# Performance work log

Measured on AMD Instinct MI355X. Metric: run time of the kernel, lower is better.

Reference implementation:

```python
import jax, jax.numpy as jnp
import numpy as np

D, IN_CH, H, W = 4, 13, 384, 384
EMBED, HID, N_COLORS = 64, 32, 11


def conv(x, w, b, stride=1, pad=0):
    y = jax.lax.conv_general_dilated(
        x, w, window_strides=(stride, stride),
        padding=[(pad, pad), (pad, pad)],
        dimension_numbers=('NCHW', 'OIHW', 'NCHW'))
    return y + b[None, :, None, None]


def setup_inputs() -> dict:
    key = jax.random.key(0)
    ks = jax.random.split(key, 16)
    s = 0.05
    return {
        'demo_inputs': jax.random.normal(ks[0], (D, IN_CH, H, W), jnp.float32),
        'demo_outputs': jax.random.normal(ks[1], (D, IN_CH, H, W), jnp.float32),
        'test_input': jax.random.normal(ks[2], (IN_CH, H, W), jnp.float32),
        'enc_w1': jax.random.normal(ks[3], (32, 26, 3, 3), jnp.float32) * s,
        'enc_b1': jnp.zeros((32,), jnp.float32),
        'enc_w2': jax.random.normal(ks[4], (64, 32, 3, 3), jnp.float32) * s,
        'enc_b2': jnp.zeros((64,), jnp.float32),
        'enc_w3': jax.random.normal(ks[5], (64, 64, 3, 3), jnp.float32) * s,
        'enc_b3': jnp.zeros((64,), jnp.float32),
        'enc_lw': jax.random.normal(ks[6], (EMBED, 64), jnp.float32) * s,
        'enc_lb': jnp.zeros((EMBED,), jnp.float32),
        'stem_w': jax.random.normal(ks[7], (HID, IN_CH, 3, 3), jnp.float32) * s,
        'stem_b': jnp.zeros((HID,), jnp.float32),
        'upd_w1': jax.random.normal(ks[8], (HID, HID + EMBED, 3, 3), jnp.float32) * s,
        'upd_b1': jnp.zeros((HID,), jnp.float32),
        'upd_w2': jax.random.normal(ks[9], (HID, HID, 1, 1), jnp.float32) * s,
        'upd_b2': jnp.zeros((HID,), jnp.float32),
        'tau_w': jax.random.normal(ks[10], (HID, HID + EMBED, 1, 1), jnp.float32) * s,
        'tau_b': jnp.zeros((HID,), jnp.float32),
        'dec_w': jax.random.normal(ks[11], (N_COLORS, HID, 1, 1), jnp.float32) * s,
        'dec_b': jnp.zeros((N_COLORS,), jnp.float32),
        'n_steps': 8,
    }


def reference(demo_inputs, demo_outputs, test_input,
              enc_w1, enc_b1, enc_w2, enc_b2, enc_w3, enc_b3, enc_lw, enc_lb,
              stem_w, stem_b, upd_w1, upd_b1, upd_w2, upd_b2,
              tau_w, tau_b, dec_w, dec_b, n_steps):
    # encode_demos: concat each (in, out) pair along channels -> [D, 2*in_ch, H, W]
    pairs = jnp.concatenate([demo_inputs, demo_outputs], axis=1)
    h = jax.nn.relu(conv(pairs, enc_w1, enc_b1, stride=1, pad=1))
    h = jax.nn.relu(conv(h, enc_w2, enc_b2, stride=2, pad=1))
    h = jax.nn.relu(conv(h, enc_w3, enc_b3, stride=2, pad=1))
    h = h.mean(axis=(2, 3))                      # AdaptiveAvgPool2d(1) + Flatten -> [D, 64]
    emb = h @ enc_lw.T + enc_lb                  # [D, embed_dim]
    task_embed = emb.mean(axis=0)                # [embed_dim]

    x = test_input[None]                         # [1, in_ch, H, W]
    Hh, Ww = x.shape[2], x.shape[3]
    te = jnp.broadcast_to(task_embed[None, :, None, None], (1, task_embed.shape[0], Hh, Ww))
    state = jax.nn.relu(conv(x, stem_w, stem_b, stride=1, pad=1))
    for _ in range(n_steps):
        ctx = jnp.concatenate([state, te], axis=1)   # [1, hid+embed, H, W]
        delta = conv(jax.nn.relu(conv(ctx, upd_w1, upd_b1, stride=1, pad=1)),
                     upd_w2, upd_b2, stride=1, pad=0)
        beta = jax.nn.sigmoid(conv(ctx, tau_w, tau_b, stride=1, pad=0))
        state = beta * state + (1.0 - beta) * delta
    return conv(state, dec_w, dec_b, stride=1, pad=0)  # [1, N_COLORS, H, W]
```

## Files before the change

### kernel.cpp

```cpp
#include <hip/hip_runtime.h>

#define HW 147456

typedef __attribute__((ext_vector_type(8))) short bf16x8;
typedef __attribute__((ext_vector_type(4))) float f32x4;

__device__ __forceinline__ float bf2f(unsigned short u) {
    return __uint_as_float(((unsigned)u) << 16);
}
__device__ __forceinline__ unsigned short f2bf(float f) {
    unsigned u = __float_as_uint(f);
    return (unsigned short)((u + 0x7fffu + ((u >> 16) & 1u)) >> 16);
}

struct TJobs {
    const float* src[5];
    float* dst[5];
    int cout[5], cintot[5], k[5], coutp[5];
    int start[6];
};

__global__ __launch_bounds__(256) void transpose_all_k(TJobs J) {
    int gid = blockIdx.x * 256 + threadIdx.x;
    if (gid >= J.start[5]) return;
    int j = 0;
#pragma unroll
    for (int t = 1; t < 5; ++t)
        if (gid >= J.start[t]) j = t;
    int li = gid - J.start[j];
    int coutp = J.coutp[j], K = J.k[j];
    int co = li % coutp;
    int kk = (li / coutp) % K;
    int cin = li / (coutp * K);
    J.dst[j][li] = (co < J.cout[j]) ? J.src[j][((co * J.cintot[j]) + cin) * K + kk] : 0.f;
}

struct WJobs {
    const float* src[4];
    unsigned short* dst[4];
    int cout[4], cin[4], cintot[4], cinp[4];
    int start[5];
};

__global__ __launch_bounds__(256) void transpose_wbf_k(WJobs J) {
    int gid = blockIdx.x * 256 + threadIdx.x;
    if (gid >= J.start[4]) return;
    int j = 0;
#pragma unroll
    for (int t = 1; t < 4; ++t)
        if (gid >= J.start[t]) j = t;
    int li = gid - J.start[j];
    int cinp = J.cinp[j];
    int ci = li % cinp;
    int co = (li / cinp) % J.cout[j];
    int tap = li / (cinp * J.cout[j]);
    float v = (ci < J.cin[j]) ? J.src[j][((co * J.cintot[j]) + ci) * 9 + tap] : 0.f;
    J.dst[j][li] = f2bf(v);
}

template <int CIN, int CP, int COUT, int S, int OX, int OY, int MW, bool RELU>
__global__ __launch_bounds__(256, MW) void mfma_conv_k(
    const float* __restrict__ in0, const float* __restrict__ in1, int split,
    long off0base, long off1base, long zs0, long zs1, int inW, int inH,
    const unsigned short* __restrict__ wB,
    const float* __restrict__ bias,
    float* __restrict__ out, long outZS) {
    constexpr int XT = (OX - 1) * S + 3;
    constexpr int YT = (OY - 1) * S + 3;
    constexpr int CINK = (CIN + 31) & ~31;
    constexpr int KST = CINK / 32;
    constexpr int NCG = COUT / 16;
    constexpr int NTX = OX / 16;
    constexpr int NSP = NTX * OY;
    constexpr int NTASK = NSP * NCG;
    constexpr int NT4 = NTASK / 4;
    constexpr int NSLOT = YT * XT;
    static_assert(NTASK % 4 == 0, "tasks per wave");
    static_assert(NSP % NT4 == 0, "wave must own a single cout-group");
    static_assert(CP % 8 == 0 && CP >= CINK, "LDS cin pad");
    static_assert((CP / 8) % 2 == 1, "odd chunk stride for bank spread");
    __shared__ __align__(16) unsigned short tile[NSLOT * CP];
    const int tid = threadIdx.x;
    const int bx = blockIdx.x, by = blockIdx.y, z = blockIdx.z;
    const long o0 = off0base + (long)z * zs0;
    const long o1 = off1base + (long)z * zs1;
    const int outW = inW / S, outH = inH / S;
    const int gx0 = bx * OX * S - 1;
    const int gy0 = by * OY * S - 1;

#pragma unroll 1
    for (int s = tid; s < NSLOT; s += 256) {
        const int sy = s / XT;
        const int lx = s - sy * XT;
        const int gy = gy0 + sy;
        const int gx = gx0 + lx;
        const bool ok = ((unsigned)gy < (unsigned)inH) && ((unsigned)gx < (unsigned)inW);
        const long pix = (long)gy * inW + gx;
#pragma unroll
        for (int h = 0; h < CINK / 8; ++h) {
            bf16x8 v;
#pragma unroll
            for (int e = 0; e < 8; ++e) {
                const int c = h * 8 + e;
                float f = 0.f;
                if (c < CIN && ok) {
                    const float* base = (c < split)
                        ? in0 + o0 + (long)c * inH * inW
                        : in1 + o1 + (long)(c - split) * inH * inW;
                    f = base[pix];
                }
                v[e] = (short)f2bf(f);
            }
            *(bf16x8*)(tile + s * CP + h * 8) = v;
        }
    }
    __syncthreads();

    const int wv = tid >> 6;
    const int l = tid & 63;
    const int ln = l & 15;
    const int lk = l >> 4;
    const int cg = (wv * NT4) / NSP;
    bf16x8 bfr[9 * KST];
#pragma unroll
    for (int tap = 0; tap < 9; ++tap)
#pragma unroll
        for (int h = 0; h < KST; ++h)
            bfr[tap * KST + h] = *(const bf16x8*)(wB + ((long)(tap * COUT + cg * 16 + ln)) * CINK + h * 32 + lk * 8);
    const float bv = bias[cg * 16 + ln];
#pragma unroll 1
    for (int t = 0; t < NT4; ++t) {
        const int sp = wv * NT4 + t - cg * NSP;
        const int tx = sp % NTX;
        const int ty = sp / NTX;
        f32x4 acc;
        acc[0] = bv; acc[1] = bv; acc[2] = bv; acc[3] = bv;
#pragma unroll
        for (int ky = 0; ky < 3; ++ky) {
#pragma unroll
            for (int kx = 0; kx < 3; ++kx) {
                const int yb = ty * S + ky;
                const int xb = (tx * 16 + ln) * S + kx;
                const unsigned short* ap = tile + (yb * XT + xb) * CP + lk * 8;
#pragma unroll
                for (int h = 0; h < KST; ++h) {
                    bf16x8 a = *(const bf16x8*)(ap + h * 32);
                    acc = __builtin_amdgcn_mfma_f32_16x16x32_bf16(a, bfr[(ky * 3 + kx) * KST + h], acc, 0, 0, 0);
                }
            }
        }
        const int ox = bx * OX + tx * 16 + lk * 4;
        const int oy = by * OY + ty;
        float4 o;
        if constexpr (RELU) {
            o.x = fmaxf(acc[0], 0.f);
            o.y = fmaxf(acc[1], 0.f);
            o.z = fmaxf(acc[2], 0.f);
            o.w = fmaxf(acc[3], 0.f);
        } else {
            o.x = acc[0]; o.y = acc[1]; o.z = acc[2]; o.w = acc[3];
        }
        *(float4*)(out + (long)z * outZS + ((long)(cg * 16 + ln) * outH + oy) * outW + ox) = o;
    }
}

template <int CIN, int CCHUNK, int WCH, int COUT, int STRIDE, int TW, int CO_PER, int MW>
__global__ __launch_bounds__(256, MW) void conv3x3_k(
    const float* __restrict__ in0, const float* __restrict__ in1, int split,
    long inOff0, long inOff1, long zs0, long zs1, int inW, int inH,
    const float* __restrict__ wT, const float* __restrict__ bias,
    float* __restrict__ out, long outZS) {
    constexpr int NCG = COUT / CO_PER;
    constexpr int NPXG = 256 / NCG;
    constexpr int NXG = TW / 4;
    constexpr int TH = NPXG / NXG;
    constexpr int INW = (TW - 1) * STRIDE + 3;
    constexpr int INH = (TH - 1) * STRIDE + 3;
    constexpr int WIN = 3 * STRIDE + 3;
    constexpr int XV = (INW + 6) / 4;
    constexpr int LDSW = XV * 4 + 1;
    constexpr int SLOTS = INH * XV;
    static_assert(NPXG % NXG == 0 && NPXG * NCG == 256, "thread mapping");
    static_assert(CIN % CCHUNK == 0 && CCHUNK % WCH == 0, "chunking");
    static_assert(SLOTS <= 256, "staging slots");
    __shared__ float tile[CCHUNK][INH][LDSW];
    __shared__ __align__(16) float wlds[WCH * 9 * COUT];
    const int tid = threadIdx.x;
    const int cg = tid / NPXG;
    const int pg = tid % NPXG;
    const int xg = pg % NXG;
    const int yy = pg / NXG;
    const int bx = blockIdx.x, by = blockIdx.y, z = blockIdx.z;
    const int outW = inW / STRIDE, outH = inH / STRIDE;
    const long off0 = inOff0 + (long)z * zs0;
    const long off1 = inOff1 + (long)z * zs1;
    float* outp = out + (long)z * outZS;
    const bool sact = tid < SLOTS;
    const int sr = tid / XV;
    const int sx = tid - sr * XV;
    const int gxs = bx * TW * STRIDE - 4 + sx * 4;
    const int gy0 = by * TH * STRIDE - 1;

    float acc[4][CO_PER];
    {
        float bv[CO_PER];
#pragma unroll
        for (int jj = 0; jj < CO_PER; jj += 4) {
            float4 b4 = *(const float4*)(bias + cg * CO_PER + jj);
            bv[jj] = b4.x; bv[jj + 1] = b4.y; bv[jj + 2] = b4.z; bv[jj + 3] = b4.w;
        }
#pragma unroll
        for (int p = 0; p < 4; ++p)
#pragma unroll
            for (int j = 0; j < CO_PER; ++j) acc[p][j] = bv[j];
    }

    for (int ch = 0; ch < CIN; ch += CCHUNK) {
        if (sact) {
            const int gy = gy0 + sr;
            const bool yok = (unsigned)gy < (unsigned)inH;
            const bool xfull = (gxs >= 0) && (gxs + 3 < inW);
#pragma unroll
            for (int c = 0; c < CCHUNK; ++c) {
                const int gc = ch + c;
                const float* row = (gc < split)
                    ? in0 + off0 + ((long)gc * inH + gy) * inW
                    : in1 + off1 + ((long)(gc - split) * inH + gy) * inW;
                float4 v = {0.f, 0.f, 0.f, 0.f};
                if (yok) {
                    if (xfull) {
                        v = *(const float4*)(row + gxs);
                    } else {
                        float t[4];
#pragma unroll
                        for (int k = 0; k < 4; ++k) {
                            int gx = gxs + k;
                            t[k] = ((unsigned)gx < (unsigned)inW) ? row[gx] : 0.f;
                        }
                        v = {t[0], t[1], t[2], t[3]};
                    }
                }
                float* dst = &tile[c][sr][sx * 4];
                dst[0] = v.x; dst[1] = v.y; dst[2] = v.z; dst[3] = v.w;
            }
        }
#pragma unroll 1
        for (int wc = 0; wc < CCHUNK; wc += WCH) {
            {
                const float4* wsrc = (const float4*)(wT + (long)(ch + wc) * 9 * COUT);
                float4* wdst = (float4*)wlds;
                constexpr int CNT = WCH * 9 * COUT / 4;
                for (int i = tid; i < CNT; i += 256) wdst[i] = wsrc[i];
            }
            __syncthreads();
#pragma unroll 1
            for (int c = 0; c < WCH; ++c) {
#pragma unroll
                for (int ky = 0; ky < 3; ++ky) {
                    const int ty = yy * STRIDE + ky;
                    const int tx0 = xg * 4 * STRIDE + 3;
                    float xw[WIN];
#pragma unroll
                    for (int i = 0; i < WIN; ++i) xw[i] = tile[wc + c][ty][tx0 + i];
#pragma unroll
                    for (int dx = 0; dx < 3; ++dx) {
                        const float* wp = wlds + ((c * 3 + ky) * 3 + dx) * COUT + cg * CO_PER;
                        float wv[CO_PER];
#pragma unroll
                        for (int jj = 0; jj < CO_PER; jj += 4) {
                            float4 w4 = *(const float4*)(wp + jj);
                            wv[jj] = w4.x; wv[jj + 1] = w4.y; wv[jj + 2] = w4.z; wv[jj + 3] = w4.w;
                        }
#pragma unroll
                        for (int p = 0; p < 4; ++p) {
                            float xv = xw[p * STRIDE + dx];
#pragma unroll
                            for (int j = 0; j < CO_PER; ++j) acc[p][j] = fmaf(xv, wv[j], acc[p][j]);
                        }
                    }
                }
            }
            __syncthreads();
        }
    }

    const int ox0 = bx * TW + xg * 4;
    const int oy = by * TH + yy;
#pragma unroll
    for (int j = 0; j < CO_PER; ++j) {
        int co = cg * CO_PER + j;
        float4 o;
        o.x = fmaxf(acc[0][j], 0.f);
        o.y = fmaxf(acc[1][j], 0.f);
        o.z = fmaxf(acc[2][j], 0.f);
        o.w = fmaxf(acc[3][j], 0.f);
        *(float4*)(outp + ((long)co * outH + oy) * outW + ox0) = o;
    }
}

__global__ __launch_bounds__(256) void pool_k(const float* __restrict__ enc3base,
                                              long zstride,
                                              float* __restrict__ meanout) {
    int z = blockIdx.x >> 6;
    int c = blockIdx.x & 63;
    const float* p = enc3base + (long)z * zstride + (long)c * 9216;
    float s = 0.f;
    for (int i = threadIdx.x; i < 9216; i += 256) s += p[i];
    __shared__ float red[256];
    red[threadIdx.x] = s;
    __syncthreads();
    for (int o = 128; o > 0; o >>= 1) {
        if (threadIdx.x < o) red[threadIdx.x] += red[threadIdx.x + o];
        __syncthreads();
    }
    if (threadIdx.x == 0) meanout[z * 64 + c] = red[0] * (1.f / 9216.f);
}

__global__ __launch_bounds__(256) void prep_te_k(
    const float* __restrict__ means, const float* __restrict__ lw,
    const float* __restrict__ lb, const float* __restrict__ tauw,
    const float* __restrict__ taub, const float* __restrict__ w1,
    const float* __restrict__ b1,
    float* __restrict__ tauc, float* __restrict__ wsum,
    float* __restrict__ bias2) {
    __shared__ float tes[64];
    int t = threadIdx.x;
    if (t < 64) {
        float s = 0.f;
        for (int d = 0; d < 4; ++d)
            for (int c = 0; c < 64; ++c) s += means[d * 64 + c] * lw[t * 64 + c];
        tes[t] = lb[t] + 0.25f * s;
    }
    __syncthreads();
    if (t < 32) {
        float s = taub[t];
        for (int e = 0; e < 64; ++e) s += tauw[t * 96 + 32 + e] * tes[e];
        tauc[t] = s;
    }
    for (int i = t; i < 288; i += 256) {
        int co = i % 32;
        int k = i / 32;
        float s = 0.f;
        for (int e = 0; e < 64; ++e) s += w1[((co * 96) + 32 + e) * 9 + k] * tes[e];
        wsum[i] = s;
    }
    __syncthreads();
    if (t < 32) {
        float s = b1[t];
        for (int k = 0; k < 9; ++k) s += wsum[k * 32 + t];
        bias2[t] = s;
    }
}

__global__ __launch_bounds__(256, 4) void nca_fuse_k(
    const float* __restrict__ sold, float* __restrict__ hb,
    const float* __restrict__ wsum, const float* __restrict__ w2T,
    const float* __restrict__ b2, const float* __restrict__ tauT,
    const float* __restrict__ tauc) {
    __shared__ unsigned short h1s[32][136];
    __shared__ __align__(16) float ss[32][132];
    __shared__ __align__(16) float sw2[1024];
    __shared__ __align__(16) float stu[1024];
    __shared__ float swv[288], sb2[32], stc[32];
    const int tid = threadIdx.x;
    const long px0 = (long)blockIdx.x * 128;
    for (int i = tid; i < 1024; i += 256) {
        sw2[i] = w2T[i];
        stu[i] = tauT[i];
    }
    for (int i = tid; i < 288; i += 256) swv[i] = wsum[i];
    if (tid < 32) {
        sb2[tid] = b2[tid];
        stc[tid] = tauc[tid];
    }
    const int yrow = (int)(px0 / 384);
    const int xbase = (int)(px0 - (long)yrow * 384);
    const bool ytop = (yrow == 0), ybot = (yrow == 383);
#pragma unroll 1
    for (int i = tid; i < 1024; i += 256) {
        const int ch = i >> 5;
        const int p4 = i & 31;
        float4 h4 = *(const float4*)(hb + (long)ch * HW + px0 + p4 * 4);
        float4 s4 = *(const float4*)(sold + (long)ch * HW + px0 + p4 * 4);
        float hv[4] = {h4.x, h4.y, h4.z, h4.w};
        unsigned short ho[4];
#pragma unroll
        for (int e = 0; e < 4; ++e) {
            const int x = xbase + p4 * 4 + e;
            float h = hv[e];
            const bool xl = (x == 0), xr = (x == 383);
            if (xl | xr | ytop | ybot) {
#pragma unroll
                for (int ky = 0; ky < 3; ++ky)
#pragma unroll
                    for (int kx = 0; kx < 3; ++kx) {
                        bool inval = (ky == 0 && ytop) || (ky == 2 && ybot) ||
                                     (kx == 0 && xl) || (kx == 2 && xr);
                        if (inval) h -= swv[(ky * 3 + kx) * 32 + ch];
                    }
            }
            ho[e] = f2bf(fmaxf(h, 0.f));
        }
        unsigned short* hd = &h1s[ch][p4 * 4];
        hd[0] = ho[0]; hd[1] = ho[1]; hd[2] = ho[2]; hd[3] = ho[3];
        *(float4*)(&ss[ch][p4 * 4]) = s4;
    }
    __syncthreads();

    const int cg = tid >> 5;
    const int pg = tid & 31;
    const int p0 = pg * 4;
    float accd[4][4], acct[4][4];
    {
        float dv[4], tv[4];
#pragma unroll
        for (int j = 0; j < 4; ++j) {
            dv[j] = sb2[cg * 4 + j];
            tv[j] = stc[cg * 4 + j];
        }
#pragma unroll
        for (int p = 0; p < 4; ++p)
#pragma unroll
            for (int j = 0; j < 4; ++j) { accd[p][j] = dv[j]; acct[p][j] = tv[j]; }
    }
#pragma unroll 2
    for (int ci = 0; ci < 32; ++ci) {
        float hv[4], sv[4];
#pragma unroll
        for (int p = 0; p < 4; ++p) {
            hv[p] = bf2f(h1s[ci][p0 + p]);
            sv[p] = ss[ci][p0 + p];
        }
        float4 wd4 = *(const float4*)(sw2 + ci * 32 + cg * 4);
        float4 wt4 = *(const float4*)(stu + ci * 32 + cg * 4);
        float wdv[4] = {wd4.x, wd4.y, wd4.z, wd4.w};
        float wtv[4] = {wt4.x, wt4.y, wt4.z, wt4.w};
#pragma unroll
        for (int p = 0; p < 4; ++p) {
#pragma unroll
            for (int j = 0; j < 4; ++j) {
                accd[p][j] = fmaf(hv[p], wdv[j], accd[p][j]);
                acct[p][j] = fmaf(sv[p], wtv[j], acct[p][j]);
            }
        }
    }
#pragma unroll
    for (int j = 0; j < 4; ++j) {
        const int co = cg * 4 + j;
        float ov[4];
#pragma unroll
        for (int p = 0; p < 4; ++p) {
            float sown = ss[co][p0 + p];
            float beta = 1.f / (1.f + __expf(-acct[p][j]));
            ov[p] = beta * sown + (1.f - beta) * accd[p][j];
        }
        float4 o = {ov[0], ov[1], ov[2], ov[3]};
        *(float4*)(hb + (long)co * HW + px0 + p0) = o;
    }
}

__global__ __launch_bounds__(256) void dec_k(const float* __restrict__ st,
                                             const float* __restrict__ dT,
                                             const float* __restrict__ db,
                                             float* __restrict__ out) {
    int gid = blockIdx.x * 256 + threadIdx.x;
    long px0 = (long)gid * 2;
    float acc[11][2];
#pragma unroll
    for (int co = 0; co < 11; ++co) {
        float b = db[co];
        acc[co][0] = b;
        acc[co][1] = b;
    }
    for (int ci = 0; ci < 32; ++ci) {
        float2 s2 = *(const float2*)(st + (long)ci * HW + px0);
        const float* wp = dT + ci * 12;
        float4 w0 = *(const float4*)wp, w1 = *(const float4*)(wp + 4), w2 = *(const float4*)(wp + 8);
        float wv[12] = {w0.x, w0.y, w0.z, w0.w, w1.x, w1.y, w1.z, w1.w, w2.x, w2.y, w2.z, w2.w};
#pragma unroll
        for (int co = 0; co < 11; ++co) {
            acc[co][0] = fmaf(s2.x, wv[co], acc[co][0]);
            acc[co][1] = fmaf(s2.y, wv[co], acc[co][1]);
        }
    }
#pragma unroll
    for (int co = 0; co < 11; ++co) {
        float2 o = {acc[co][0], acc[co][1]};
        *(float2*)(out + (long)co * HW + px0) = o;
    }
}

extern "C" void kernel_launch(void* const* d_in, const int* in_sizes, int n_in,
                              void* d_out, int out_size, void* d_ws, size_t ws_size,
                              hipStream_t stream) {
    float* out = (float*)d_out;
    const float* demo_in = (const float*)d_in[0];
    const float* demo_out = (const float*)d_in[1];
    const float* test_in = (const float*)d_in[2];
    const float* enc_w1 = (const float*)d_in[3];
    const float* enc_b1 = (const float*)d_in[4];
    const float* enc_w2 = (const float*)d_in[5];
    const float* enc_b2 = (const float*)d_in[6];
    const float* enc_w3 = (const float*)d_in[7];
    const float* enc_b3 = (const float*)d_in[8];
    const float* enc_lw = (const float*)d_in[9];
    const float* enc_lb = (const float*)d_in[10];
    const float* stem_w = (const float*)d_in[11];
    const float* stem_b = (const float*)d_in[12];
    const float* upd_w1 = (const float*)d_in[13];
    const float* upd_b1 = (const float*)d_in[14];
    const float* upd_w2 = (const float*)d_in[15];
    const float* upd_b2 = (const float*)d_in[16];
    const float* tau_w = (const float*)d_in[17];
    const float* tau_b = (const float*)d_in[18];
    const float* dec_w = (const float*)d_in[19];
    const float* dec_b = (const float*)d_in[20];

    float* Wb = (float*)d_ws;
    float* wT_D = Wb + 0;
    float* w2T  = Wb + 3744;
    float* tauT = Wb + 4768;
    float* decT = Wb + 5792;
    float* tauc = Wb + 6176;
    float* wsum = Wb + 6208;
    float* means = Wb + 6496;
    float* bias2 = Wb + 6752;
    unsigned short* wB1 = (unsigned short*)(Wb + 6784);
    unsigned short* wB2 = (unsigned short*)(Wb + 11392);
    unsigned short* wB3 = (unsigned short*)(Wb + 20608);
    unsigned short* wBE = (unsigned short*)(Wb + 39040);
    float* big = Wb + 45056;

    const long PD = 7667712;
    const long E1 = 4718592, E2 = 2359296;
    size_t wsf = ws_size / 4;
    int NZ = 1;
    if (wsf >= 45056 + 4 * (size_t)PD) NZ = 4;
    else if (wsf >= 45056 + 2 * (size_t)PD) NZ = 2;

    TJobs J;
    {
        const float* srcs[5] = {stem_w, upd_w2, tau_w, dec_w, dec_w};
        float* dsts[5] = {wT_D, w2T, tauT, decT, decT};
        int couts[5] = {32, 32, 32, 11, 0};
        int cintots[5] = {13, 32, 96, 32, 32};
        int ks[5] = {9, 1, 1, 1, 1};
        int cinsels[5] = {13, 32, 32, 32, 0};
        int coutps[5] = {32, 32, 32, 12, 12};
        int acc0 = 0;
        for (int j = 0; j < 5; ++j) {
            J.src[j] = srcs[j]; J.dst[j] = dsts[j];
            J.cout[j] = couts[j]; J.cintot[j] = cintots[j];
            J.k[j] = ks[j]; J.coutp[j] = coutps[j];
            J.start[j] = acc0;
            acc0 += cinsels[j] * ks[j] * coutps[j];
        }
        J.start[5] = acc0;
        transpose_all_k<<<(acc0 + 255) / 256, 256, 0, stream>>>(J);
    }
    WJobs W;
    {
        const float* srcs[4] = {enc_w1, enc_w2, enc_w3, upd_w1};
        unsigned short* dsts[4] = {wB1, wB2, wB3, wBE};
        int couts[4] = {32, 64, 64, 32};
        int cins[4] = {26, 32, 64, 32};
        int cintots[4] = {26, 32, 64, 96};
        int cinps[4] = {32, 32, 64, 32};
        int acc0 = 0;
        for (int j = 0; j < 4; ++j) {
            W.src[j] = srcs[j]; W.dst[j] = dsts[j];
            W.cout[j] = couts[j]; W.cin[j] = cins[j];
            W.cintot[j] = cintots[j]; W.cinp[j] = cinps[j];
            W.start[j] = acc0;
            acc0 += 9 * couts[j] * cinps[j];
        }
        W.start[4] = acc0;
        transpose_wbf_k<<<(acc0 + 255) / 256, 256, 0, stream>>>(W);
    }

    for (int d0 = 0; d0 < 4; d0 += NZ) {
        mfma_conv_k<26, 40, 32, 1, 64, 4, 5, true><<<dim3(6, 96, NZ), 256, 0, stream>>>(
            demo_in, demo_out, 13, (long)d0 * 13 * HW, (long)d0 * 13 * HW,
            13L * HW, 13L * HW, 384, 384, wB1, enc_b1, big, PD);
        mfma_conv_k<32, 40, 64, 2, 32, 2, 5, true><<<dim3(6, 96, NZ), 256, 0, stream>>>(
            big, big, 32, 0, 0, PD, PD, 384, 384, wB2, enc_b2, big + E1, PD);
        mfma_conv_k<64, 72, 64, 2, 16, 2, 5, true><<<dim3(6, 48, NZ), 256, 0, stream>>>(
            big + E1, big + E1, 64, 0, 0, PD, PD, 192, 192, wB3, enc_b3,
            big + E1 + E2, PD);
        pool_k<<<64 * NZ, 256, 0, stream>>>(big + E1 + E2, PD, means + d0 * 64);
    }
    prep_te_k<<<1, 256, 0, stream>>>(means, enc_lw, enc_lb, tau_w, tau_b, upd_w1,
                                     upd_b1, tauc, wsum, bias2);

    float* sA = big;
    float* sX = big + E1;
    conv3x3_k<13, 13, 13, 32, 1, 32, 8, 5><<<dim3(12, 48, 1), 256, 0, stream>>>(
        test_in, test_in, 13, 0, 0, 0, 0, 384, 384, wT_D, stem_b, sA, 0);

    float* a = sA;
    float* b = sX;
    for (int s = 0; s < 8; ++s) {
        mfma_conv_k<32, 40, 32, 1, 32, 8, 5, false><<<dim3(12, 48, 1), 256, 0, stream>>>(
            a, a, 32, 0, 0, 0, 0, 384, 384, wBE, bias2, b, 0);
        nca_fuse_k<<<1152, 256, 0, stream>>>(a, b, wsum, w2T, upd_b2, tauT, tauc);
        float* t = a; a = b; b = t;
    }
    dec_k<<<288, 256, 0, stream>>>(a, decT, dec_b, out);
}
```

Measured before the change: 504.4 us.

## Fuse NCA 3x3 MFMA conv and 1x1 update into one per-step kernel

```diff
diff --git a/kernel.cpp b/kernel.cpp
--- a/kernel.cpp
+++ b/kernel.cpp
@@ -352,62 +352,123 @@
     }
 }
 
-__global__ __launch_bounds__(256, 4) void nca_fuse_k(
-    const float* __restrict__ sold, float* __restrict__ hb,
-    const float* __restrict__ wsum, const float* __restrict__ w2T,
-    const float* __restrict__ b2, const float* __restrict__ tauT,
-    const float* __restrict__ tauc) {
-    __shared__ unsigned short h1s[32][136];
+__global__ __launch_bounds__(256, 2) void nca_step_fused_k(
+    const float* __restrict__ sold, float* __restrict__ snew,
+    const unsigned short* __restrict__ wBE,
+    const float* __restrict__ bias2,
+    const float* __restrict__ wsum,
+    const float* __restrict__ w2T, const float* __restrict__ b2,
+    const float* __restrict__ tauT, const float* __restrict__ tauc) {
+    __shared__ __align__(16) unsigned short tile[204 * 40];
     __shared__ __align__(16) float ss[32][132];
-    __shared__ __align__(16) float sw2[1024];
-    __shared__ __align__(16) float stu[1024];
-    __shared__ float swv[288], sb2[32], stc[32];
+    __shared__ __align__(16) float sw2[1024], stu[1024];
+    __shared__ float sb2[32], stc[32];
     const int tid = threadIdx.x;
-    const long px0 = (long)blockIdx.x * 128;
+    const int bx = blockIdx.x, by = blockIdx.y;
+    const int gx0 = bx * 32 - 1;
+    const int gy0 = by * 4 - 1;
+
     for (int i = tid; i < 1024; i += 256) {
         sw2[i] = w2T[i];
         stu[i] = tauT[i];
     }
-    for (int i = tid; i < 288; i += 256) swv[i] = wsum[i];
     if (tid < 32) {
         sb2[tid] = b2[tid];
         stc[tid] = tauc[tid];
     }
-    const int yrow = (int)(px0 / 384);
-    const int xbase = (int)(px0 - (long)yrow * 384);
-    const bool ytop = (yrow == 0), ybot = (yrow == 383);
-#pragma unroll 1
-    for (int i = tid; i < 1024; i += 256) {
-        const int ch = i >> 5;
-        const int p4 = i & 31;
-        float4 h4 = *(const float4*)(hb + (long)ch * HW + px0 + p4 * 4);
-        float4 s4 = *(const float4*)(sold + (long)ch * HW + px0 + p4 * 4);
-        float hv[4] = {h4.x, h4.y, h4.z, h4.w};
-        unsigned short ho[4];
-#pragma unroll
-        for (int e = 0; e < 4; ++e) {
-            const int x = xbase + p4 * 4 + e;
-            float h = hv[e];
-            const bool xl = (x == 0), xr = (x == 383);
+    if (tid < 204) {
+        const int sy = tid / 34;
+        const int lx = tid - sy * 34;
+        const int gy = gy0 + sy;
+        const int gx = gx0 + lx;
+        const bool ok = ((unsigned)gy < 384u) && ((unsigned)gx < 384u);
+        const long pix = (long)gy * 384 + gx;
+        const bool ctr = (sy >= 1) && (sy <= 4) && (lx >= 1) && (lx <= 32);
+        const int pxl = (sy - 1) * 32 + (lx - 1);
+#pragma unroll
+        for (int h = 0; h < 4; ++h) {
+            bf16x8 v;
+#pragma unroll
+            for (int e = 0; e < 8; ++e) {
+                const int c = h * 8 + e;
+                float f = ok ? sold[(long)c * HW + pix] : 0.f;
+                v[e] = (short)f2bf(f);
+                if (ctr) ss[c][pxl] = f;
+            }
+            *(bf16x8*)(tile + tid * 40 + h * 8) = v;
+        }
+    }
+    __syncthreads();
+
+    const int wv = tid >> 6;
+    const int l = tid & 63;
+    const int ln = l & 15;
+    const int lk = l >> 4;
+    const int cg = wv >> 1;
+    const int co = cg * 16 + ln;
+    bf16x8 bfr[9];
+#pragma unroll
+    for (int tap = 0; tap < 9; ++tap)
+        bfr[tap] = *(const bf16x8*)(wBE + ((long)(tap * 32 + co)) * 32 + lk * 8);
+    const float bv = bias2[co];
+    f32x4 accs[4];
+#pragma unroll
+    for (int t = 0; t < 4; ++t) {
+        const int sp = (wv & 1) * 4 + t;
+        const int tx = sp & 1;
+        const int ty = sp >> 1;
+        f32x4 acc;
+        acc[0] = bv; acc[1] = bv; acc[2] = bv; acc[3] = bv;
+#pragma unroll
+        for (int ky = 0; ky < 3; ++ky) {
+#pragma unroll
+            for (int kx = 0; kx < 3; ++kx) {
+                const unsigned short* ap = tile + ((ty + ky) * 34 + tx * 16 + ln + kx) * 40 + lk * 8;
+                bf16x8 a = *(const bf16x8*)ap;
+                acc = __builtin_amdgcn_mfma_f32_16x16x32_bf16(a, bfr[ky * 3 + kx], acc, 0, 0, 0);
+            }
+        }
+        accs[t] = acc;
+    }
+    __syncthreads();
+
+    unsigned short (*h1s)[136] = (unsigned short(*)[136])tile;
+#pragma unroll
+    for (int t = 0; t < 4; ++t) {
+        const int sp = (wv & 1) * 4 + t;
+        const int tx = sp & 1;
+        const int ty = sp >> 1;
+        const int gy = by * 4 + ty;
+        const int gxb = bx * 32 + tx * 16 + lk * 4;
+        float hv[4] = {accs[t][0], accs[t][1], accs[t][2], accs[t][3]};
+        const bool ytop = (gy == 0), ybot = (gy == 383);
+#pragma unroll
+        for (int r = 0; r < 4; ++r) {
+            const int gx = gxb + r;
+            const bool xl = (gx == 0), xr = (gx == 383);
             if (xl | xr | ytop | ybot) {
+                float h = hv[r];
 #pragma unroll
                 for (int ky = 0; ky < 3; ++ky)
 #pragma unroll
                     for (int kx = 0; kx < 3; ++kx) {
                         bool inval = (ky == 0 && ytop) || (ky == 2 && ybot) ||
                                      (kx == 0 && xl) || (kx == 2 && xr);
-                        if (inval) h -= swv[(ky * 3 + kx) * 32 + ch];
+                        if (inval) h -= wsum[(ky * 3 + kx) * 32 + co];
                     }
-            }
-            ho[e] = f2bf(fmaxf(h, 0.f));
-        }
-        unsigned short* hd = &h1s[ch][p4 * 4];
-        hd[0] = ho[0]; hd[1] = ho[1]; hd[2] = ho[2]; hd[3] = ho[3];
-        *(float4*)(&ss[ch][p4 * 4]) = s4;
+                hv[r] = h;
+            }
+        }
+        ushort4 ho;
+        ho.x = f2bf(fmaxf(hv[0], 0.f));
+        ho.y = f2bf(fmaxf(hv[1], 0.f));
+        ho.z = f2bf(fmaxf(hv[2], 0.f));
+        ho.w = f2bf(fmaxf(hv[3], 0.f));
+        *(ushort4*)(&h1s[co][ty * 32 + tx * 16 + lk * 4]) = ho;
     }
     __syncthreads();
 
-    const int cg = tid >> 5;
+    const int cg2 = tid >> 5;
     const int pg = tid & 31;
     const int p0 = pg * 4;
     float accd[4][4], acct[4][4];
@@ -415,8 +476,8 @@
         float dv[4], tv[4];
 #pragma unroll
         for (int j = 0; j < 4; ++j) {
-            dv[j] = sb2[cg * 4 + j];
-            tv[j] = stc[cg * 4 + j];
+            dv[j] = sb2[cg2 * 4 + j];
+            tv[j] = stc[cg2 * 4 + j];
         }
 #pragma unroll
         for (int p = 0; p < 4; ++p)
@@ -431,8 +492,8 @@
             hv[p] = bf2f(h1s[ci][p0 + p]);
             sv[p] = ss[ci][p0 + p];
         }
-        float4 wd4 = *(const float4*)(sw2 + ci * 32 + cg * 4);
-        float4 wt4 = *(const float4*)(stu + ci * 32 + cg * 4);
+        float4 wd4 = *(const float4*)(sw2 + ci * 32 + cg2 * 4);
+        float4 wt4 = *(const float4*)(stu + ci * 32 + cg2 * 4);
         float wdv[4] = {wd4.x, wd4.y, wd4.z, wd4.w};
         float wtv[4] = {wt4.x, wt4.y, wt4.z, wt4.w};
 #pragma unroll
@@ -444,18 +505,21 @@
             }
         }
     }
+    const int yl = p0 >> 5;
+    const int xl2 = p0 & 31;
+    const long obase = ((long)(by * 4 + yl)) * 384 + bx * 32 + xl2;
 #pragma unroll
     for (int j = 0; j < 4; ++j) {
-        const int co = cg * 4 + j;
+        const int co2 = cg2 * 4 + j;
         float ov[4];
 #pragma unroll
         for (int p = 0; p < 4; ++p) {
-            float sown = ss[co][p0 + p];
+            float sown = ss[co2][p0 + p];
             float beta = 1.f / (1.f + __expf(-acct[p][j]));
             ov[p] = beta * sown + (1.f - beta) * accd[p][j];
         }
         float4 o = {ov[0], ov[1], ov[2], ov[3]};
-        *(float4*)(hb + (long)co * HW + px0 + p0) = o;
+        *(float4*)(snew + (long)co2 * HW + obase) = o;
     }
 }
 
@@ -600,9 +664,8 @@
     float* a = sA;
     float* b = sX;
     for (int s = 0; s < 8; ++s) {
-        mfma_conv_k<32, 40, 32, 1, 32, 8, 5, false><<<dim3(12, 48, 1), 256, 0, stream>>>(
-            a, a, 32, 0, 0, 0, 0, 384, 384, wBE, bias2, b, 0);
-        nca_fuse_k<<<1152, 256, 0, stream>>>(a, b, wsum, w2T, upd_b2, tauT, tauc);
+        nca_step_fused_k<<<dim3(12, 96), 256, 0, stream>>>(
+            a, b, wBE, bias2, wsum, w2T, upd_b2, tauT, tauc);
         float* t = a; a = b; b = t;
     }
     dec_k<<<288, 256, 0, stream>>>(a, decT, dec_b, out);
```

After: 490.3 us. 1.03x faster.
